# Optimization experiments

Hardware: AMD Instinct MI355X
Metric: run time of the kernel (lower is better)

## Reference

```python
import jax, jax.numpy as jnp
import numpy as np

N_NODES = 20000
N_EDGES = 320000
IN_CH = 256
HID = 128
HEADS = 4
OUT_CH = 200
NUM_GRAPHS = 64
NEG_SLOPE = 0.2


def setup_inputs() -> dict:
    key = jax.random.key(0)
    ks = jax.random.split(key, 16)
    x = jax.random.normal(ks[0], (N_NODES, IN_CH), dtype=jnp.float32)
    edge_index = jax.random.randint(ks[1], (2, N_EDGES), 0, N_NODES, dtype=jnp.int64)
    batch = jnp.sort(jax.random.randint(ks[2], (N_NODES,), 0, NUM_GRAPHS, dtype=jnp.int64))

    def lin(k, fan_in, fan_out):
        return jax.random.normal(k, (fan_in, fan_out), dtype=jnp.float32) / np.sqrt(fan_in)

    def att(k, h, c):
        return jax.random.normal(k, (h, c), dtype=jnp.float32) / np.sqrt(c)

    return {
        "x": x, "edge_index": edge_index, "batch": batch,
        "W1": lin(ks[3], IN_CH, HEADS * HID),
        "a_src1": att(ks[4], HEADS, HID), "a_dst1": att(ks[5], HEADS, HID),
        "b1": jnp.zeros((HEADS * HID,), jnp.float32),
        "W2": lin(ks[6], HEADS * HID, HEADS * HID),
        "a_src2": att(ks[7], HEADS, HID), "a_dst2": att(ks[8], HEADS, HID),
        "b2": jnp.zeros((HEADS * HID,), jnp.float32),
        "W3": lin(ks[9], HEADS * HID, HID),
        "a_src3": att(ks[10], 1, HID), "a_dst3": att(ks[11], 1, HID),
        "b3": jnp.zeros((HID,), jnp.float32),
        "fc_w": lin(ks[12], HID, OUT_CH),
        "fc_b": jnp.zeros((OUT_CH,), jnp.float32),
    }


def gat_conv(x, src, dst, W, a_src, a_dst, bias):
    """PyG GATConv (concat=True, negative_slope=0.2, self-loops appended by caller)."""
    N = x.shape[0]
    heads, out_ch = a_src.shape
    h = (x @ W).reshape(N, heads, out_ch)                 # [N,H,C]
    alpha_s = jnp.einsum('nhc,hc->nh', h, a_src)          # [N,H]
    alpha_d = jnp.einsum('nhc,hc->nh', h, a_dst)
    e = jax.nn.leaky_relu(alpha_s[src] + alpha_d[dst], NEG_SLOPE)  # [E,H]
    # segment softmax over edges sharing the same target node
    m = jax.ops.segment_max(e, dst, num_segments=N)
    e = jnp.exp(e - m[dst])
    denom = jax.ops.segment_sum(e, dst, num_segments=N)
    alpha = e / (denom[dst] + 1e-16)                      # [E,H]
    msg = h[src] * alpha[:, :, None]                      # [E,H,C]
    out = jax.ops.segment_sum(msg, dst, num_segments=N)   # [N,H,C]
    return out.reshape(N, heads * out_ch) + bias


def reference(x, edge_index, batch, W1, a_src1, a_dst1, b1,
              W2, a_src2, a_dst2, b2, W3, a_src3, a_dst3, b3, fc_w, fc_b):
    N = x.shape[0]
    loop = jnp.arange(N, dtype=edge_index.dtype)
    src = jnp.concatenate([edge_index[0], loop])
    dst = jnp.concatenate([edge_index[1], loop])

    h = jax.nn.elu(gat_conv(x, src, dst, W1, a_src1, a_dst1, b1))
    h = jax.nn.elu(gat_conv(h, src, dst, W2, a_src2, a_dst2, b2))
    h = jax.nn.elu(gat_conv(h, src, dst, W3, a_src3, a_dst3, b3))

    # global_mean_pool over graph ids
    sums = jax.ops.segment_sum(h, batch, num_segments=NUM_GRAPHS)
    cnts = jax.ops.segment_sum(jnp.ones((N,), h.dtype), batch, num_segments=NUM_GRAPHS)
    pooled = sums / jnp.maximum(cnts, 1.0)[:, None]       # [G,HID]
    # F.dropout with training=False is identity
    logits = pooled @ fc_w + fc_b                          # [G,OUT_CH]
    return logits
```

## Files before the change

kernel.cpp:

```cpp
#include <hip/hip_runtime.h>
#include <hip/hip_bf16.h>
#include <stdint.h>

#define N_NODES   20000
#define N_EDGES   320000
#define E_TOT     (N_EDGES + N_NODES)
#define IN_CH     256
#define HID       128
#define HEADS     4
#define OUT_CH    200
#define NUM_GRAPHS 64
#define M_PAD     20096

typedef __bf16 bf16_t;
typedef __bf16 bf16x8 __attribute__((ext_vector_type(8)));
typedef __bf16 bf16x2 __attribute__((ext_vector_type(2)));
typedef float  f32x4  __attribute__((ext_vector_type(4)));

__device__ __forceinline__ bool detect_bf16(const unsigned short* __restrict__ xu16) {
  int lane = threadIdx.x & 63;
  unsigned short v = xu16[2 * lane];
  int e = (v >> 7) & 0xff;
  unsigned long long b = __ballot(e >= 90 && e <= 160);
  return __popcll(b) >= 40;
}
__device__ __forceinline__ bool detect_i64(const unsigned* __restrict__ eidx) {
  int lane = threadIdx.x & 63;
  unsigned long long b = __ballot(eidx[2 * lane + 1] == 0u);
  return __popcll(b) >= 32;
}

__global__ void cvt_x(const void* __restrict__ src, bf16_t* __restrict__ dst, int n,
                      const unsigned short* __restrict__ xu16,
                      float* __restrict__ psums) {
  bool isbf = detect_bf16(xu16);
  int i = blockIdx.x * 256 + threadIdx.x;
  if (i < NUM_GRAPHS * HID) psums[i] = 0.f;
  if (i >= n) return;
  dst[i] = isbf ? ((const bf16_t*)src)[i] : (bf16_t)((const float*)src)[i];
}

struct SmallCvt {
  const void* src[11];
  bf16_t* dst[11];
  int n[11];
};

__global__ void cvt_wts(const void* __restrict__ W1, const void* __restrict__ W2,
                        const void* __restrict__ W3, bf16_t* __restrict__ W1T,
                        bf16_t* __restrict__ W2T, bf16_t* __restrict__ W3T,
                        SmallCvt tab, const unsigned short* __restrict__ xu16) {
  bool isbf = detect_bf16(xu16);
  int i = blockIdx.x * 256 + threadIdx.x;
  if (i < 131072) {
    int k = i >> 9, nn = i & 511;
    bf16_t v = isbf ? ((const bf16_t*)W1)[i] : (bf16_t)((const float*)W1)[i];
    W1T[(size_t)nn * 256 + k] = v;
  } else if (i < 131072 + 262144) {
    int i2 = i - 131072;
    int k = i2 >> 9, nn = i2 & 511;
    bf16_t v = isbf ? ((const bf16_t*)W2)[i2] : (bf16_t)((const float*)W2)[i2];
    W2T[(size_t)nn * 512 + k] = v;
  } else if (i < 131072 + 262144 + 65536) {
    int i3 = i - 131072 - 262144;
    int k = i3 >> 7, nn = i3 & 127;
    bf16_t v = isbf ? ((const bf16_t*)W3)[i3] : (bf16_t)((const float*)W3)[i3];
    W3T[(size_t)nn * 512 + k] = v;
  } else {
    int j = i - 458752;
    for (int s = 0; s < 11; ++s) {
      if (j < tab.n[s]) {
        tab.dst[s][j] = isbf ? ((const bf16_t*)tab.src[s])[j]
                             : (bf16_t)((const float*)tab.src[s])[j];
        break;
      }
      j -= tab.n[s];
    }
  }
}

__global__ void cvt_ints_hist(const int* __restrict__ eidx, const int* __restrict__ batch,
                              int* __restrict__ esrc, int* __restrict__ edst,
                              int* __restrict__ b32, int* __restrict__ deg,
                              const unsigned* __restrict__ eidx_u) {
  bool i64 = detect_i64(eidx_u);
  int i = blockIdx.x * 256 + threadIdx.x;
  if (i < N_EDGES) {
    int s = i64 ? eidx[2 * i] : eidx[i];
    int d = i64 ? eidx[2 * (N_EDGES + i)] : eidx[N_EDGES + i];
    esrc[i] = s;
    edst[i] = d;
    atomicAdd(&deg[d], 1);
  }
  if (i < N_NODES) {
    b32[i] = i64 ? batch[2 * i] : batch[i];
    atomicAdd(&deg[i], 1);
  }
}

__launch_bounds__(1024)
__global__ void scan_deg(const int* __restrict__ deg, int* __restrict__ off,
                         int* __restrict__ cursor) {
  __shared__ int wsum[16];
  __shared__ int carry_s;
  int t = threadIdx.x;
  int lane = t & 63, wid = t >> 6;
  if (t == 0) { carry_s = 0; off[0] = 0; }
  __syncthreads();
  for (int base = 0; base < N_NODES; base += 1024) {
    int i = base + t;
    int v = (i < N_NODES) ? deg[i] : 0;
    int x = v;
    for (int d = 1; d < 64; d <<= 1) {
      int y = __shfl_up(x, d);
      if (lane >= d) x += y;
    }
    if (lane == 63) wsum[wid] = x;
    __syncthreads();
    if (t < 16) {
      int y = wsum[t];
      for (int d = 1; d < 16; d <<= 1) {
        int z = __shfl_up(y, d);
        if (t >= d) y += z;
      }
      wsum[t] = y;
    }
    __syncthreads();
    int carry = carry_s;
    int prefix = (wid > 0 ? wsum[wid - 1] : 0) + carry;
    int incl = prefix + x;
    if (i < N_NODES) { off[i + 1] = incl; cursor[i] = 0; }
    __syncthreads();
    if (t == 0) carry_s = carry + wsum[15];
    __syncthreads();
  }
}

__global__ void scatter_kernel(const int* __restrict__ esrc, const int* __restrict__ edst,
                               const int* __restrict__ off, int* __restrict__ cursor,
                               int* __restrict__ csr_src) {
  int e = blockIdx.x * 256 + threadIdx.x;
  if (e >= E_TOT) return;
  int s, d;
  if (e < N_EDGES) { s = esrc[e]; d = edst[e]; } else { s = d = e - N_EDGES; }
  int pos = off[d] + atomicAdd(&cursor[d], 1);
  csr_src[pos] = s;
}

__launch_bounds__(256)
__global__ void gemm_bf16(const bf16_t* __restrict__ A, const bf16_t* __restrict__ BT,
                          bf16_t* __restrict__ C, int M, int N, int K) {
  __shared__ bf16_t As[128 * 32];
  __shared__ bf16_t Bs[128 * 32];
  const int tid  = threadIdx.x;
  const int lane = tid & 63;
  const int w    = tid >> 6;
  const int wm   = w & 1, wn = w >> 1;
  const int bm   = blockIdx.x * 128;
  const int bn   = blockIdx.y * 128;
  const int quad = lane >> 4;
  const int l16  = lane & 15;

  f32x4 zero = {0.f, 0.f, 0.f, 0.f};
  f32x4 acc[4][4];
  for (int i = 0; i < 4; ++i)
    for (int j = 0; j < 4; ++j) acc[i][j] = zero;

  const int c0 = tid, c1 = tid + 256;
  const int r0 = c0 >> 2, s0 = c0 & 3;
  const int r1 = c1 >> 2, s1 = c1 & 3;
  int ga0 = bm + r0; if (ga0 > M - 1) ga0 = M - 1;
  int ga1 = bm + r1; if (ga1 > M - 1) ga1 = M - 1;

  for (int k0 = 0; k0 < K; k0 += 32) {
    bf16x8 va0 = *(const bf16x8*)(A + (size_t)ga0 * K + k0 + s0 * 8);
    bf16x8 vb0 = *(const bf16x8*)(BT + (size_t)(bn + r0) * K + k0 + s0 * 8);
    bf16x8 va1 = *(const bf16x8*)(A + (size_t)ga1 * K + k0 + s1 * 8);
    bf16x8 vb1 = *(const bf16x8*)(BT + (size_t)(bn + r1) * K + k0 + s1 * 8);
    __syncthreads();
    *(bf16x8*)(As + c0 * 8) = va0;
    *(bf16x8*)(Bs + c0 * 8) = vb0;
    *(bf16x8*)(As + c1 * 8) = va1;
    *(bf16x8*)(Bs + c1 * 8) = vb1;
    __syncthreads();

    bf16x8 af[4], bfr[4];
    for (int mt = 0; mt < 4; ++mt) {
      int m_local = wm * 64 + mt * 16 + l16;
      af[mt] = *(const bf16x8*)(As + m_local * 32 + quad * 8);
    }
    for (int nt = 0; nt < 4; ++nt) {
      int n_local = wn * 64 + nt * 16 + l16;
      bfr[nt] = *(const bf16x8*)(Bs + n_local * 32 + quad * 8);
    }
    for (int mt = 0; mt < 4; ++mt)
      for (int nt = 0; nt < 4; ++nt)
        acc[mt][nt] = __builtin_amdgcn_mfma_f32_16x16x32_bf16(af[mt], bfr[nt], acc[mt][nt], 0, 0, 0);
  }

  for (int mt = 0; mt < 4; ++mt) {
    for (int r = 0; r < 4; ++r) {
      int m = bm + wm * 64 + mt * 16 + quad * 4 + r;
      if (m >= M) continue;
      for (int nt = 0; nt < 4; ++nt) {
        int n = bn + wn * 64 + nt * 16 + l16;
        C[(size_t)m * N + n] = (bf16_t)acc[mt][nt][r];
      }
    }
  }
}

template<int CPL>
__launch_bounds__(256)
__global__ void alpha_k(const bf16_t* __restrict__ h, const bf16_t* __restrict__ a_src,
                        const bf16_t* __restrict__ a_dst, float* __restrict__ as,
                        float* __restrict__ ad, int H) {
  typedef __bf16 vec_t __attribute__((ext_vector_type(CPL)));
  const int C = CPL * 64;
  int lane = threadIdx.x & 63;
  int n = blockIdx.x * 4 + (threadIdx.x >> 6);
  if (n >= N_NODES) return;
  int c0 = lane * CPL;
  vec_t hv  = *(const vec_t*)(h + (size_t)n * C + c0);
  vec_t sv  = *(const vec_t*)(a_src + c0);
  vec_t dv  = *(const vec_t*)(a_dst + c0);
  float s = 0.f, d = 0.f;
  for (int j = 0; j < CPL; ++j) {
    float hvf = (float)hv[j];
    s += hvf * (float)sv[j];
    d += hvf * (float)dv[j];
  }
  const int lph = 128 / CPL;
  for (int o = 1; o < lph; o <<= 1) {
    s += __shfl_xor(s, o);
    d += __shfl_xor(d, o);
  }
  if ((lane & (lph - 1)) == 0) {
    int hd = c0 >> 7;
    as[n * H + hd] = s;
    ad[n * H + hd] = d;
  }
}

template<int CPL>
__launch_bounds__(256)
__global__ void agg_fused(const bf16_t* __restrict__ h, const int* __restrict__ off,
                          const int* __restrict__ csr_src, const float* __restrict__ as,
                          const float* __restrict__ ad, const bf16_t* __restrict__ bias,
                          bf16_t* __restrict__ outp, int H) {
  typedef __bf16 vec_t __attribute__((ext_vector_type(CPL)));
  const int C = CPL * 64;
  int lane = threadIdx.x & 63;
  int n = blockIdx.x * 4 + (threadIdx.x >> 6);
  if (n >= N_NODES) return;
  int start = __builtin_amdgcn_readfirstlane(off[n]);
  int end   = __builtin_amdgcn_readfirstlane(off[n + 1]);
  int c0 = lane * CPL;
  int hd = c0 >> 7;
  float adv = ad[n * H + hd];
  float acc[CPL];
  for (int j = 0; j < CPL; ++j) acc[j] = 0.f;
  float den = 0.f;

  int pos = start;
  for (; pos + 1 < end; pos += 2) {
    int s0 = __builtin_amdgcn_readfirstlane(csr_src[pos]);
    int s1 = __builtin_amdgcn_readfirstlane(csr_src[pos + 1]);
    vec_t hv0 = *(const vec_t*)(h + (size_t)s0 * C + c0);
    vec_t hv1 = *(const vec_t*)(h + (size_t)s1 * C + c0);
    float e0 = as[s0 * H + hd] + adv; e0 = e0 > 0.f ? e0 : 0.2f * e0;
    float e1 = as[s1 * H + hd] + adv; e1 = e1 > 0.f ? e1 : 0.2f * e1;
    float w0 = __expf(e0), w1 = __expf(e1);
    den += w0 + w1;
    for (int j = 0; j < CPL; ++j)
      acc[j] += w0 * (float)hv0[j] + w1 * (float)hv1[j];
  }
  if (pos < end) {
    int s0 = __builtin_amdgcn_readfirstlane(csr_src[pos]);
    vec_t hv0 = *(const vec_t*)(h + (size_t)s0 * C + c0);
    float e0 = as[s0 * H + hd] + adv; e0 = e0 > 0.f ? e0 : 0.2f * e0;
    float w0 = __expf(e0);
    den += w0;
    for (int j = 0; j < CPL; ++j) acc[j] += w0 * (float)hv0[j];
  }

  float inv = 1.f / (den + 1e-16f);
  vec_t ov;
  for (int j = 0; j < CPL; ++j) {
    float o = acc[j] * inv + (float)bias[c0 + j];
    o = o > 0.f ? o : expm1f(o);
    ov[j] = (bf16_t)o;
  }
  *(vec_t*)(outp + (size_t)n * C + c0) = ov;
}

__launch_bounds__(256)
__global__ void pool_partial(const bf16_t* __restrict__ h3, const int* __restrict__ batch,
                             float* __restrict__ psums) {
  int wave = threadIdx.x >> 6;
  int lane = threadIdx.x & 63;
  int c0 = lane * 2;
  int nbase = blockIdx.x * 128;
  int nend = nbase + 128; if (nend > N_NODES) nend = N_NODES;
  float a0 = 0.f, a1 = 0.f;
  int cur = -1;
  for (int n = nbase + wave; n < nend; n += 4) {
    int g = __builtin_amdgcn_readfirstlane(batch[n]);
    if (g != cur) {
      if (cur >= 0) {
        atomicAdd(&psums[cur * HID + c0], a0);
        atomicAdd(&psums[cur * HID + c0 + 1], a1);
      }
      cur = g; a0 = 0.f; a1 = 0.f;
    }
    bf16x2 v = *(const bf16x2*)(h3 + (size_t)n * HID + c0);
    a0 += (float)v[0];
    a1 += (float)v[1];
  }
  if (cur >= 0) {
    atomicAdd(&psums[cur * HID + c0], a0);
    atomicAdd(&psums[cur * HID + c0 + 1], a1);
  }
}

__launch_bounds__(256)
__global__ void fc_final(const float* __restrict__ psums, const int* __restrict__ batch,
                         const bf16_t* __restrict__ fcw, const bf16_t* __restrict__ fcb,
                         void* __restrict__ outp, const unsigned short* __restrict__ xu16) {
  bool isbf = detect_bf16(xu16);
  int g = blockIdx.x;
  int lo = 0, hi = N_NODES;
  while (lo < hi) { int mid = (lo + hi) >> 1; if (batch[mid] < g) lo = mid + 1; else hi = mid; }
  int start = lo;
  hi = N_NODES;
  while (lo < hi) { int mid = (lo + hi) >> 1; if (batch[mid] < g + 1) lo = mid + 1; else hi = mid; }
  int cnt = lo - start;
  __shared__ float pooled[HID];
  int t = threadIdx.x;
  if (t < HID) {
    pooled[t] = psums[g * HID + t] / (float)(cnt > 0 ? cnt : 1);
  }
  __syncthreads();
  if (t < OUT_CH) {
    float a = (float)fcb[t];
    for (int c = 0; c < HID; ++c) a += pooled[c] * (float)fcw[c * OUT_CH + t];
    if (isbf) ((bf16_t*)outp)[g * OUT_CH + t] = (bf16_t)a;
    else      ((float*)outp)[g * OUT_CH + t] = a;
  }
}

extern "C" void kernel_launch(void* const* d_in, const int* in_sizes, int n_in,
                              void* d_out, int out_size, void* d_ws, size_t ws_size,
                              hipStream_t stream) {
  const void* x    = d_in[0];
  const void* eidx = d_in[1];
  const void* batch= d_in[2];
  const void* W1   = d_in[3];
  const void* a_s1 = d_in[4];
  const void* a_d1 = d_in[5];
  const void* b1   = d_in[6];
  const void* W2   = d_in[7];
  const void* a_s2 = d_in[8];
  const void* a_d2 = d_in[9];
  const void* b2   = d_in[10];
  const void* W3   = d_in[11];
  const void* a_s3 = d_in[12];
  const void* a_d3 = d_in[13];
  const void* b3   = d_in[14];
  const void* fcw  = d_in[15];
  const void* fcb  = d_in[16];
  const unsigned short* xu16 = (const unsigned short*)x;

  char* p = (char*)d_ws;
  auto carve = [&](size_t nbytes) { char* r = p; p += (nbytes + 255) & ~(size_t)255; return r; };
  bf16_t*   W1T    = (bf16_t*)carve((size_t)512 * 256 * 2);
  bf16_t*   W2T    = (bf16_t*)carve((size_t)512 * 512 * 2);
  bf16_t*   W3T    = (bf16_t*)carve((size_t)128 * 512 * 2);
  bf16_t*   hA     = (bf16_t*)carve((size_t)M_PAD * 512 * 2);
  bf16_t*   hB     = (bf16_t*)carve((size_t)M_PAD * 512 * 2);
  bf16_t*   xb     = hB;
  bf16_t*   sm     = (bf16_t*)carve((size_t)32768 * 2);
  bf16_t *as1b = sm, *ad1b = sm + 512, *b1b = sm + 1024,
         *as2b = sm + 1536, *ad2b = sm + 2048, *b2b = sm + 2560,
         *as3b = sm + 3072, *ad3b = sm + 3200, *b3b = sm + 3328,
         *fcwb = sm + 3456, *fcbb = sm + 29056;
  float*    asb    = (float*)carve((size_t)N_NODES * 4 * 4);
  float*    adb    = (float*)carve((size_t)N_NODES * 4 * 4);
  int*      deg    = (int*)carve((size_t)N_NODES * 4);
  int*      off    = (int*)carve((size_t)(N_NODES + 1) * 4);
  int*      cursor = (int*)carve((size_t)N_NODES * 4);
  int*      csr_src= (int*)carve((size_t)E_TOT * 4);
  int*      esrc32 = (int*)carve((size_t)N_EDGES * 4);
  int*      edst32 = (int*)carve((size_t)N_EDGES * 4);
  int*      bat32  = (int*)carve((size_t)N_NODES * 4);
  float*    psums  = (float*)carve((size_t)NUM_GRAPHS * HID * 4);

  dim3 b256(256);
  const int NG4 = (N_NODES + 3) / 4;

  hipMemsetAsync(deg, 0, (size_t)N_NODES * 4, stream);
  cvt_x<<<dim3((N_NODES * IN_CH + 255) / 256), b256, 0, stream>>>(x, xb, N_NODES * IN_CH,
                                                                  xu16, psums);
  SmallCvt tab;
  const void* srcs[11] = {a_s1, a_d1, b1, a_s2, a_d2, b2, a_s3, a_d3, b3, fcw, fcb};
  bf16_t* dsts[11] = {as1b, ad1b, b1b, as2b, ad2b, b2b, as3b, ad3b, b3b, fcwb, fcbb};
  int ns[11] = {512, 512, 512, 512, 512, 512, 128, 128, 128, 25600, 200};
  for (int i = 0; i < 11; ++i) { tab.src[i] = srcs[i]; tab.dst[i] = dsts[i]; tab.n[i] = ns[i]; }
  cvt_wts<<<dim3((458752 + 29256 + 255) / 256), b256, 0, stream>>>(W1, W2, W3, W1T, W2T, W3T, tab, xu16);
  cvt_ints_hist<<<dim3((N_EDGES + 255) / 256), b256, 0, stream>>>(
      (const int*)eidx, (const int*)batch, esrc32, edst32, bat32, deg, (const unsigned*)eidx);

  scan_deg<<<dim3(1), dim3(1024), 0, stream>>>(deg, off, cursor);
  scatter_kernel<<<dim3((E_TOT + 255) / 256), b256, 0, stream>>>(esrc32, edst32, off, cursor, csr_src);

  gemm_bf16<<<dim3(157, 4), b256, 0, stream>>>(xb, W1T, hA, N_NODES, 512, 256);
  alpha_k<8><<<dim3(NG4), b256, 0, stream>>>(hA, as1b, ad1b, asb, adb, 4);
  agg_fused<8><<<dim3(NG4), b256, 0, stream>>>(hA, off, csr_src, asb, adb, b1b, hB, 4);

  gemm_bf16<<<dim3(157, 4), b256, 0, stream>>>(hB, W2T, hA, N_NODES, 512, 512);
  alpha_k<8><<<dim3(NG4), b256, 0, stream>>>(hA, as2b, ad2b, asb, adb, 4);
  agg_fused<8><<<dim3(NG4), b256, 0, stream>>>(hA, off, csr_src, asb, adb, b2b, hB, 4);

  gemm_bf16<<<dim3(157, 1), b256, 0, stream>>>(hB, W3T, hA, N_NODES, 128, 512);
  alpha_k<2><<<dim3(NG4), b256, 0, stream>>>(hA, as3b, ad3b, asb, adb, 1);
  agg_fused<2><<<dim3(NG4), b256, 0, stream>>>(hA, off, csr_src, asb, adb, b3b, hB, 1);

  pool_partial<<<dim3((N_NODES + 127) / 128), b256, 0, stream>>>(hB, bat32, psums);
  fc_final<<<dim3(NUM_GRAPHS), b256, 0, stream>>>(psums, bat32, fcwb, fcbb, d_out, xu16);
}
```

Measured before the change: 380.3 us.

## Fuse x conversion into GEMM, fold memset, single-wave scan, unroll aggregation

Drops the separate fp32-to-bf16 conversion kernel for x and has the first GEMM load fp32 rows and convert them in registers. The degree memset and psums zeroing move into cvt_wts. The 1024-thread block scan is replaced by a single-wave scan in which each lane handles a serial segment. The aggregation edge loop is unrolled from two to four neighbours. Together these remove two launches and the intermediate x buffer round trip, at the cost of a wider fp32 A-load in the first GEMM, a serial per-lane scan, and more registers in the aggregation loop.

```diff
diff --git a/kernel.cpp b/kernel.cpp
--- a/kernel.cpp
+++ b/kernel.cpp
@@ -30,16 +30,6 @@
   return __popcll(b) >= 32;
 }
 
-__global__ void cvt_x(const void* __restrict__ src, bf16_t* __restrict__ dst, int n,
-                      const unsigned short* __restrict__ xu16,
-                      float* __restrict__ psums) {
-  bool isbf = detect_bf16(xu16);
-  int i = blockIdx.x * 256 + threadIdx.x;
-  if (i < NUM_GRAPHS * HID) psums[i] = 0.f;
-  if (i >= n) return;
-  dst[i] = isbf ? ((const bf16_t*)src)[i] : (bf16_t)((const float*)src)[i];
-}
-
 struct SmallCvt {
   const void* src[11];
   bf16_t* dst[11];
@@ -49,9 +39,12 @@
 __global__ void cvt_wts(const void* __restrict__ W1, const void* __restrict__ W2,
                         const void* __restrict__ W3, bf16_t* __restrict__ W1T,
                         bf16_t* __restrict__ W2T, bf16_t* __restrict__ W3T,
-                        SmallCvt tab, const unsigned short* __restrict__ xu16) {
+                        SmallCvt tab, const unsigned short* __restrict__ xu16,
+                        int* __restrict__ deg, float* __restrict__ psums) {
   bool isbf = detect_bf16(xu16);
   int i = blockIdx.x * 256 + threadIdx.x;
+  if (i < N_NODES) deg[i] = 0;
+  if (i < NUM_GRAPHS * HID) psums[i] = 0.f;
   if (i < 131072) {
     int k = i >> 9, nn = i & 511;
     bf16_t v = isbf ? ((const bf16_t*)W1)[i] : (bf16_t)((const float*)W1)[i];
@@ -98,42 +91,28 @@
   }
 }
 
-__launch_bounds__(1024)
-__global__ void scan_deg(const int* __restrict__ deg, int* __restrict__ off,
-                         int* __restrict__ cursor) {
-  __shared__ int wsum[16];
-  __shared__ int carry_s;
-  int t = threadIdx.x;
-  int lane = t & 63, wid = t >> 6;
-  if (t == 0) { carry_s = 0; off[0] = 0; }
-  __syncthreads();
-  for (int base = 0; base < N_NODES; base += 1024) {
-    int i = base + t;
-    int v = (i < N_NODES) ? deg[i] : 0;
-    int x = v;
-    for (int d = 1; d < 64; d <<= 1) {
-      int y = __shfl_up(x, d);
-      if (lane >= d) x += y;
-    }
-    if (lane == 63) wsum[wid] = x;
-    __syncthreads();
-    if (t < 16) {
-      int y = wsum[t];
-      for (int d = 1; d < 16; d <<= 1) {
-        int z = __shfl_up(y, d);
-        if (t >= d) y += z;
-      }
-      wsum[t] = y;
-    }
-    __syncthreads();
-    int carry = carry_s;
-    int prefix = (wid > 0 ? wsum[wid - 1] : 0) + carry;
-    int incl = prefix + x;
-    if (i < N_NODES) { off[i + 1] = incl; cursor[i] = 0; }
-    __syncthreads();
-    if (t == 0) carry_s = carry + wsum[15];
-    __syncthreads();
-  }
+__launch_bounds__(64)
+__global__ void scan_deg_wave(const int* __restrict__ deg, int* __restrict__ off,
+                              int* __restrict__ cursor) {
+  const int SEG = 313;
+  int lane = threadIdx.x;
+  int base = lane * SEG;
+  int s = 0;
+  for (int j = 0; j < SEG; ++j) {
+    int i = base + j;
+    s += (i < N_NODES) ? deg[i] : 0;
+  }
+  int x = s;
+  for (int d = 1; d < 64; d <<= 1) {
+    int y = __shfl_up(x, d);
+    if (lane >= d) x += y;
+  }
+  int run = x - s;
+  for (int j = 0; j < SEG; ++j) {
+    int i = base + j;
+    if (i < N_NODES) { off[i] = run; run += deg[i]; cursor[i] = 0; }
+  }
+  if (lane == 63) off[N_NODES] = run;
 }
 
 __global__ void scatter_kernel(const int* __restrict__ esrc, const int* __restrict__ edst,
@@ -147,9 +126,13 @@
   csr_src[pos] = s;
 }
 
+template<bool MAYBE_F32>
 __launch_bounds__(256)
-__global__ void gemm_bf16(const bf16_t* __restrict__ A, const bf16_t* __restrict__ BT,
+__global__ void gemm_bf16(const void* __restrict__ Av, const bf16_t* __restrict__ BT,
                           bf16_t* __restrict__ C, int M, int N, int K) {
+  bool isbf = MAYBE_F32 ? detect_bf16((const unsigned short*)Av) : true;
+  const bf16_t* A  = (const bf16_t*)Av;
+  const float*  Af = (const float*)Av;
   __shared__ bf16_t As[128 * 32];
   __shared__ bf16_t Bs[128 * 32];
   const int tid  = threadIdx.x;
@@ -173,9 +156,21 @@
   int ga1 = bm + r1; if (ga1 > M - 1) ga1 = M - 1;
 
   for (int k0 = 0; k0 < K; k0 += 32) {
-    bf16x8 va0 = *(const bf16x8*)(A + (size_t)ga0 * K + k0 + s0 * 8);
+    bf16x8 va0, va1;
+    if (!MAYBE_F32 || isbf) {
+      va0 = *(const bf16x8*)(A + (size_t)ga0 * K + k0 + s0 * 8);
+      va1 = *(const bf16x8*)(A + (size_t)ga1 * K + k0 + s1 * 8);
+    } else {
+      const float* p0 = Af + (size_t)ga0 * K + k0 + s0 * 8;
+      const float* p1 = Af + (size_t)ga1 * K + k0 + s1 * 8;
+      f32x4 l0 = *(const f32x4*)p0, h0 = *(const f32x4*)(p0 + 4);
+      f32x4 l1 = *(const f32x4*)p1, h1 = *(const f32x4*)(p1 + 4);
+      for (int j = 0; j < 4; ++j) {
+        va0[j] = (bf16_t)l0[j]; va0[j + 4] = (bf16_t)h0[j];
+        va1[j] = (bf16_t)l1[j]; va1[j + 4] = (bf16_t)h1[j];
+      }
+    }
     bf16x8 vb0 = *(const bf16x8*)(BT + (size_t)(bn + r0) * K + k0 + s0 * 8);
-    bf16x8 va1 = *(const bf16x8*)(A + (size_t)ga1 * K + k0 + s1 * 8);
     bf16x8 vb1 = *(const bf16x8*)(BT + (size_t)(bn + r1) * K + k0 + s1 * 8);
     __syncthreads();
     *(bf16x8*)(As + c0 * 8) = va0;
@@ -263,19 +258,26 @@
   float den = 0.f;
 
   int pos = start;
-  for (; pos + 1 < end; pos += 2) {
+  for (; pos + 3 < end; pos += 4) {
     int s0 = __builtin_amdgcn_readfirstlane(csr_src[pos]);
     int s1 = __builtin_amdgcn_readfirstlane(csr_src[pos + 1]);
+    int s2 = __builtin_amdgcn_readfirstlane(csr_src[pos + 2]);
+    int s3 = __builtin_amdgcn_readfirstlane(csr_src[pos + 3]);
     vec_t hv0 = *(const vec_t*)(h + (size_t)s0 * C + c0);
     vec_t hv1 = *(const vec_t*)(h + (size_t)s1 * C + c0);
+    vec_t hv2 = *(const vec_t*)(h + (size_t)s2 * C + c0);
+    vec_t hv3 = *(const vec_t*)(h + (size_t)s3 * C + c0);
     float e0 = as[s0 * H + hd] + adv; e0 = e0 > 0.f ? e0 : 0.2f * e0;
     float e1 = as[s1 * H + hd] + adv; e1 = e1 > 0.f ? e1 : 0.2f * e1;
-    float w0 = __expf(e0), w1 = __expf(e1);
-    den += w0 + w1;
+    float e2 = as[s2 * H + hd] + adv; e2 = e2 > 0.f ? e2 : 0.2f * e2;
+    float e3 = as[s3 * H + hd] + adv; e3 = e3 > 0.f ? e3 : 0.2f * e3;
+    float w0 = __expf(e0), w1 = __expf(e1), w2 = __expf(e2), w3 = __expf(e3);
+    den += (w0 + w1) + (w2 + w3);
     for (int j = 0; j < CPL; ++j)
-      acc[j] += w0 * (float)hv0[j] + w1 * (float)hv1[j];
-  }
-  if (pos < end) {
+      acc[j] += (w0 * (float)hv0[j] + w1 * (float)hv1[j])
+              + (w2 * (float)hv2[j] + w3 * (float)hv3[j]);
+  }
+  for (; pos < end; ++pos) {
     int s0 = __builtin_amdgcn_readfirstlane(csr_src[pos]);
     vec_t hv0 = *(const vec_t*)(h + (size_t)s0 * C + c0);
     float e0 = as[s0 * H + hd] + adv; e0 = e0 > 0.f ? e0 : 0.2f * e0;
@@ -378,7 +380,6 @@
   bf16_t*   W3T    = (bf16_t*)carve((size_t)128 * 512 * 2);
   bf16_t*   hA     = (bf16_t*)carve((size_t)M_PAD * 512 * 2);
   bf16_t*   hB     = (bf16_t*)carve((size_t)M_PAD * 512 * 2);
-  bf16_t*   xb     = hB;
   bf16_t*   sm     = (bf16_t*)carve((size_t)32768 * 2);
   bf16_t *as1b = sm, *ad1b = sm + 512, *b1b = sm + 1024,
          *as2b = sm + 1536, *ad2b = sm + 2048, *b2b = sm + 2560,
@@ -398,30 +399,28 @@
   dim3 b256(256);
   const int NG4 = (N_NODES + 3) / 4;
 
-  hipMemsetAsync(deg, 0, (size_t)N_NODES * 4, stream);
-  cvt_x<<<dim3((N_NODES * IN_CH + 255) / 256), b256, 0, stream>>>(x, xb, N_NODES * IN_CH,
-                                                                  xu16, psums);
   SmallCvt tab;
   const void* srcs[11] = {a_s1, a_d1, b1, a_s2, a_d2, b2, a_s3, a_d3, b3, fcw, fcb};
   bf16_t* dsts[11] = {as1b, ad1b, b1b, as2b, ad2b, b2b, as3b, ad3b, b3b, fcwb, fcbb};
   int ns[11] = {512, 512, 512, 512, 512, 512, 128, 128, 128, 25600, 200};
   for (int i = 0; i < 11; ++i) { tab.src[i] = srcs[i]; tab.dst[i] = dsts[i]; tab.n[i] = ns[i]; }
-  cvt_wts<<<dim3((458752 + 29256 + 255) / 256), b256, 0, stream>>>(W1, W2, W3, W1T, W2T, W3T, tab, xu16);
+  cvt_wts<<<dim3((458752 + 29256 + 255) / 256), b256, 0, stream>>>(
+      W1, W2, W3, W1T, W2T, W3T, tab, xu16, deg, psums);
   cvt_ints_hist<<<dim3((N_EDGES + 255) / 256), b256, 0, stream>>>(
       (const int*)eidx, (const int*)batch, esrc32, edst32, bat32, deg, (const unsigned*)eidx);
 
-  scan_deg<<<dim3(1), dim3(1024), 0, stream>>>(deg, off, cursor);
+  scan_deg_wave<<<dim3(1), dim3(64), 0, stream>>>(deg, off, cursor);
   scatter_kernel<<<dim3((E_TOT + 255) / 256), b256, 0, stream>>>(esrc32, edst32, off, cursor, csr_src);
 
-  gemm_bf16<<<dim3(157, 4), b256, 0, stream>>>(xb, W1T, hA, N_NODES, 512, 256);
+  gemm_bf16<true><<<dim3(157, 4), b256, 0, stream>>>(x, W1T, hA, N_NODES, 512, 256);
   alpha_k<8><<<dim3(NG4), b256, 0, stream>>>(hA, as1b, ad1b, asb, adb, 4);
   agg_fused<8><<<dim3(NG4), b256, 0, stream>>>(hA, off, csr_src, asb, adb, b1b, hB, 4);
 
-  gemm_bf16<<<dim3(157, 4), b256, 0, stream>>>(hB, W2T, hA, N_NODES, 512, 512);
+  gemm_bf16<false><<<dim3(157, 4), b256, 0, stream>>>(hB, W2T, hA, N_NODES, 512, 512);
   alpha_k<8><<<dim3(NG4), b256, 0, stream>>>(hA, as2b, ad2b, asb, adb, 4);
   agg_fused<8><<<dim3(NG4), b256, 0, stream>>>(hA, off, csr_src, asb, adb, b2b, hB, 4);
 
-  gemm_bf16<<<dim3(157, 1), b256, 0, stream>>>(hB, W3T, hA, N_NODES, 128, 512);
+  gemm_bf16<false><<<dim3(157, 1), b256, 0, stream>>>(hB, W3T, hA, N_NODES, 128, 512);
   alpha_k<2><<<dim3(NG4), b256, 0, stream>>>(hA, as3b, ad3b, asb, adb, 1);
   agg_fused<2><<<dim3(NG4), b256, 0, stream>>>(hA, off, csr_src, asb, adb, b3b, hB, 1);
 
```

Result: slower. 417.5 us (+9.8%).
